# Performance work log

Hardware: AMD Instinct MI355X
Metric: run time of the kernel (lower is better)

Reference implementation:

```python
import jax, jax.numpy as jnp
import numpy as np


def _cubic_coeffs(t):
    # Catmull-Rom-style weights used by the original bicubic_interpolate
    t2 = t * t
    t3 = t2 * t
    cm1 = (-t3 + 2.0 * t2 - t) / 2.0
    c0 = (3.0 * t3 - 5.0 * t2 + 2.0) / 2.0
    c1 = (-3.0 * t3 + 4.0 * t2 + t) / 2.0
    c2 = 1.0 - (cm1 + c0 + c1)
    return (cm1, c0, c1, c2)


def _warp_bicubic(input_image, delta_x, delta_y):
    B, C, H, W = input_image.shape
    BXC = B * C
    # identity meshgrid, normalized to [-1, 1] then mapped back (faithful to source)
    gx = jnp.arange(W, dtype=jnp.float32)[None, None, :]   # [1,1,W]
    gy = jnp.arange(H, dtype=jnp.float32)[None, :, None]   # [1,H,1]
    new_x = 2.0 * (gx + delta_x) / max(W - 1, 1) - 1.0     # [B,H,W]
    new_y = 2.0 * (gy + delta_y) / max(H - 1, 1) - 1.0
    # un-normalize to pixel coords; tile across channels exactly like X.repeat([C,1,1,1])
    x_map = jnp.tile((new_x + 1.0) * (W - 1) / 2.0, (C, 1, 1))  # [BXC,H,W]
    y_map = jnp.tile((new_y + 1.0) * (H - 1) / 2.0, (C, 1, 1))
    x0f = jnp.floor(x_map)
    y0f = jnp.floor(y_map)
    tx = x_map - x0f
    ty = y_map - y0f
    cx = _cubic_coeffs(tx)
    cy = _cubic_coeffs(ty)
    x0 = x0f.astype(jnp.int32)
    y0 = y0f.astype(jnp.int32)
    xs = [jnp.clip(x0 + o, 0, W - 1) for o in (-1, 0, 1, 2)]
    ys = [jnp.clip(y0 + o, 0, H - 1) for o in (-1, 0, 1, 2)]
    flat = input_image.reshape(-1)                          # b-major, c-minor
    base = (jnp.arange(BXC, dtype=jnp.int32) * (H * W))[:, None, None]
    out = jnp.zeros((BXC, H, W), dtype=jnp.float32)
    for i in range(4):
        row = jnp.zeros((BXC, H, W), dtype=jnp.float32)
        off_y = base + ys[i] * W
        for j in range(4):
            row = row + cx[j] * jnp.take(flat, off_y + xs[j])  # 16-tap gather
        out = out + cy[i] * row
    return out.reshape(B, C, H, W)


def setup_inputs() -> dict:
    key = jax.random.key(0)
    k1, k2, k3 = jax.random.split(key, 3)
    B, C, H, W = 8, 3, 1024, 1024
    return {
        "input_image": jax.random.normal(k1, (B, C, H, W), dtype=jnp.float32),
        "delta_x": jax.random.normal(k2, (B, H, W), dtype=jnp.float32),
        "delta_y": jax.random.normal(k3, (B, H, W), dtype=jnp.float32),
    }


def reference(input_image, delta_x, delta_y):
    # Warp_Object.forward with flag_bicubic_or_bilinear='bicubic',
    # delta maps shared across channels (3D delta branch).
    return _warp_bicubic(input_image, delta_x, delta_y)
```

## Files before the change

kernel.cpp:

```cpp
#include <hip/hip_runtime.h>
#include <hip/hip_fp16.h>


#define RTY 7
#define RWS 30
#define RTX 8
#define CLS 80
#define STR 82
#define NQ  (RWS * (CLS / 4))

struct alignas(8) Cell {
    __half2 a;
    __half2 b;
};
struct alignas(16) Cell2 { Cell c0, c1; };

__device__ __forceinline__ void cubic_coeffs(float t, float c[4]) {
    float t2 = t * t;
    float t3 = t2 * t;
    c[0] = (-t3 + 2.0f * t2 - t) * 0.5f;
    c[1] = (3.0f * t3 - 5.0f * t2 + 2.0f) * 0.5f;
    c[2] = (-3.0f * t3 + 4.0f * t2 + t) * 0.5f;
    c[3] = 1.0f - (c[0] + c[1] + c[2]);
}

__global__ __launch_bounds__(1024, 8) void warp_bicubic_kernel(
    const float* __restrict__ img,
    const float* __restrict__ dx,
    const float* __restrict__ dy,
    float* __restrict__ out,
    int B, int C, int H, int W)
{
    __shared__ Cell lds[RWS * STR];

    const int tx = threadIdx.x;
    const int ty = threadIdx.y;
    const int tid = ty * 64 + tx;
    const int X = blockIdx.x * 64;
    const int Y = blockIdx.y * 16;
    const int db = blockIdx.z;
    const int hw = H * W;

    const int x = X + tx;
    const int y = Y + ty;
    const int pos  = y * W + x;
    const int dofs = db * hw + pos;
    const float fdx = dx[dofs];
    const float fdy = dy[dofs];

    const float* __restrict__ ch0 = img + (size_t)db * hw;
    const float* __restrict__ ch1 = img + (size_t)(db + B) * hw;
    const float* __restrict__ ch2 = img + (size_t)(db + 2 * B) * hw;

    if (tid < NQ) {
        int r  = tid / 20;
        int qc = tid - r * 20;
        int gy  = Y - RTY + r;
        int gx0 = X - RTX + 4 * qc;
        Cell cells[4];
        if (gy >= 0 && gy < H && gx0 >= 0 && gx0 <= W - 4) {
            size_t off = (size_t)gy * W + gx0;
            float4 v0 = *(const float4*)(ch0 + off);
            float4 v1 = *(const float4*)(ch1 + off);
            float4 v2 = *(const float4*)(ch2 + off);
            cells[0].a = __floats2half2_rn(v0.x, v1.x);
            cells[0].b = __floats2half2_rn(v2.x, 0.0f);
            cells[1].a = __floats2half2_rn(v0.y, v1.y);
            cells[1].b = __floats2half2_rn(v2.y, 0.0f);
            cells[2].a = __floats2half2_rn(v0.z, v1.z);
            cells[2].b = __floats2half2_rn(v2.z, 0.0f);
            cells[3].a = __floats2half2_rn(v0.w, v1.w);
            cells[3].b = __floats2half2_rn(v2.w, 0.0f);
        } else {
            int gyc = min(max(gy, 0), H - 1);
#pragma unroll
            for (int e = 0; e < 4; ++e) {
                int gxc = min(max(gx0 + e, 0), W - 1);
                size_t off = (size_t)gyc * W + gxc;
                cells[e].a = __floats2half2_rn(ch0[off], ch1[off]);
                cells[e].b = __floats2half2_rn(ch2[off], 0.0f);
            }
        }
        Cell2* dst = (Cell2*)&lds[r * STR + 4 * qc];
        dst[0] = *(const Cell2*)&cells[0];
        dst[1] = *(const Cell2*)&cells[2];
    }
    __syncthreads();

    const float xm = (float)x + fdx;
    const float ym = (float)y + fdy;
    const float x0f = floorf(xm);
    const float y0f = floorf(ym);
    const float tfx = xm - x0f;
    const float tfy = ym - y0f;

    float cx[4], cy[4];
    cubic_coeffs(tfx, cx);
    cubic_coeffs(tfy, cy);

    const int x0 = (int)x0f;
    const int y0 = (int)y0f;

    float a0, a1, a2;

    const unsigned ulx = (unsigned)(x0 - X + (RTX - 1));
    const unsigned uly = (unsigned)(y0 - Y + (RTY - 1));

    if (ulx <= (unsigned)(CLS - 4) && uly <= (unsigned)(RWS - 4)) {
        const Cell* __restrict__ base = lds + uly * STR + ulx;
        __half2 cxh[4], cyh[4];
#pragma unroll
        for (int j = 0; j < 4; ++j) {
            cxh[j] = __float2half2_rn(cx[j]);
            cyh[j] = __float2half2_rn(cy[j]);
        }
        __half2 acc01 = __float2half2_rn(0.0f);
        __half2 acc2  = __float2half2_rn(0.0f);
#pragma unroll
        for (int i = 0; i < 4; ++i) {
            const Cell* __restrict__ row = base + i * STR;
            Cell t0 = row[0];
            Cell t1 = row[1];
            Cell t2 = row[2];
            Cell t3 = row[3];
            __half2 r01 = __hmul2(cxh[0], t0.a);
            r01 = __hfma2(cxh[1], t1.a, r01);
            r01 = __hfma2(cxh[2], t2.a, r01);
            r01 = __hfma2(cxh[3], t3.a, r01);
            __half2 r2 = __hmul2(cxh[0], t0.b);
            r2 = __hfma2(cxh[1], t1.b, r2);
            r2 = __hfma2(cxh[2], t2.b, r2);
            r2 = __hfma2(cxh[3], t3.b, r2);
            acc01 = __hfma2(cyh[i], r01, acc01);
            acc2  = __hfma2(cyh[i], r2, acc2);
        }
        a0 = __low2float(acc01);
        a1 = __high2float(acc01);
        a2 = __low2float(acc2);
    } else {
        a0 = a1 = a2 = 0.0f;
        int xs[4], rowoff[4];
#pragma unroll
        for (int o = 0; o < 4; ++o) {
            xs[o] = min(max(x0 - 1 + o, 0), W - 1);
            rowoff[o] = min(max(y0 - 1 + o, 0), H - 1) * W;
        }
#pragma unroll
        for (int i = 0; i < 4; ++i) {
            float w0 = cy[i] * cx[0], w1 = cy[i] * cx[1];
            float w2 = cy[i] * cx[2], w3 = cy[i] * cx[3];
            const float* r0 = ch0 + rowoff[i];
            const float* r1 = ch1 + rowoff[i];
            const float* r2 = ch2 + rowoff[i];
            a0 = fmaf(w0, r0[xs[0]], a0); a0 = fmaf(w1, r0[xs[1]], a0);
            a0 = fmaf(w2, r0[xs[2]], a0); a0 = fmaf(w3, r0[xs[3]], a0);
            a1 = fmaf(w0, r1[xs[0]], a1); a1 = fmaf(w1, r1[xs[1]], a1);
            a1 = fmaf(w2, r1[xs[2]], a1); a1 = fmaf(w3, r1[xs[3]], a1);
            a2 = fmaf(w0, r2[xs[0]], a2); a2 = fmaf(w1, r2[xs[1]], a2);
            a2 = fmaf(w2, r2[xs[2]], a2); a2 = fmaf(w3, r2[xs[3]], a2);
        }
    }

    out[(size_t)db * hw + pos] = a0;
    out[(size_t)(db + B) * hw + pos] = a1;
    out[(size_t)(db + 2 * B) * hw + pos] = a2;
}

extern "C" void kernel_launch(void* const* d_in, const int* in_sizes, int n_in,
                              void* d_out, int out_size, void* d_ws, size_t ws_size,
                              hipStream_t stream) {
    const float* img = (const float*)d_in[0];
    const float* dx  = (const float*)d_in[1];
    const float* dy  = (const float*)d_in[2];
    float* out = (float*)d_out;

    const int B = 8, C = 3, H = 1024, W = 1024;
    dim3 block(64, 16, 1);
    dim3 grid(W / 64, H / 16, B);
    warp_bicubic_kernel<<<grid, block, 0, stream>>>(img, dx, dy, out, B, C, H, W);
}
```

Before: 63.64 us.

## Make blocks persistent over vertical tiles with double-buffered LDS prefetch

Each block now processes 8 consecutive 16-row tiles instead of one. It double-buffers the shared-memory halo tile and prefetches the next tile's image rows and displacement values into registers while the current tile is computed. The goal is to hide global load latency behind the LDS stencil math. The cost is fewer blocks (1024 instead of 8192), more registers, and a sync per tile, which may reduce occupancy and parallelism. Halo rows still get reloaded for each tile, so there is no cross-tile reuse.

```diff
diff --git a/kernel.cpp b/kernel.cpp
--- a/kernel.cpp
+++ b/kernel.cpp
@@ -2,6 +2,8 @@
 #include <hip/hip_fp16.h>
 
 
+#define TLH 16
+#define TPB 8
 #define RTY 7
 #define RWS 30
 #define RTX 8
@@ -31,139 +33,178 @@
     float* __restrict__ out,
     int B, int C, int H, int W)
 {
-    __shared__ Cell lds[RWS * STR];
+    __shared__ Cell lds[2][RWS * STR];
 
     const int tx = threadIdx.x;
     const int ty = threadIdx.y;
     const int tid = ty * 64 + tx;
-    const int X = blockIdx.x * 64;
-    const int Y = blockIdx.y * 16;
+    const int X  = blockIdx.x * 64;
+    const int Y0 = blockIdx.y * (TLH * TPB);
     const int db = blockIdx.z;
     const int hw = H * W;
-
-    const int x = X + tx;
-    const int y = Y + ty;
-    const int pos  = y * W + x;
-    const int dofs = db * hw + pos;
-    const float fdx = dx[dofs];
-    const float fdy = dy[dofs];
 
     const float* __restrict__ ch0 = img + (size_t)db * hw;
     const float* __restrict__ ch1 = img + (size_t)(db + B) * hw;
     const float* __restrict__ ch2 = img + (size_t)(db + 2 * B) * hw;
 
-    if (tid < NQ) {
-        int r  = tid / 20;
-        int qc = tid - r * 20;
-        int gy  = Y - RTY + r;
-        int gx0 = X - RTX + 4 * qc;
-        Cell cells[4];
-        if (gy >= 0 && gy < H && gx0 >= 0 && gx0 <= W - 4) {
-            size_t off = (size_t)gy * W + gx0;
-            float4 v0 = *(const float4*)(ch0 + off);
-            float4 v1 = *(const float4*)(ch1 + off);
-            float4 v2 = *(const float4*)(ch2 + off);
-            cells[0].a = __floats2half2_rn(v0.x, v1.x);
-            cells[0].b = __floats2half2_rn(v2.x, 0.0f);
-            cells[1].a = __floats2half2_rn(v0.y, v1.y);
-            cells[1].b = __floats2half2_rn(v2.y, 0.0f);
-            cells[2].a = __floats2half2_rn(v0.z, v1.z);
-            cells[2].b = __floats2half2_rn(v2.z, 0.0f);
-            cells[3].a = __floats2half2_rn(v0.w, v1.w);
-            cells[3].b = __floats2half2_rn(v2.w, 0.0f);
+    const int x = X + tx;
+
+    const bool sact = tid < NQ;
+    const int sr   = tid / 20;
+    const int sqc  = tid - sr * 20;
+    const int sgx0 = X - RTX + 4 * sqc;
+
+    float4 v0, v1, v2;
+    float fdx_n, fdy_n;
+
+    auto issue_delta = [&](int t) {
+        int y = Y0 + t * TLH + ty;
+        int dofs = db * hw + y * W + x;
+        fdx_n = dx[dofs];
+        fdy_n = dy[dofs];
+    };
+
+    auto issue_stage = [&](int t) {
+        if (!sact) return;
+        int gy = Y0 + t * TLH - RTY + sr;
+        if (gy >= 0 && gy < H && sgx0 >= 0 && sgx0 <= W - 4) {
+            size_t off = (size_t)gy * W + sgx0;
+            v0 = *(const float4*)(ch0 + off);
+            v1 = *(const float4*)(ch1 + off);
+            v2 = *(const float4*)(ch2 + off);
         } else {
             int gyc = min(max(gy, 0), H - 1);
+            float e0[4], e1[4], e2[4];
 #pragma unroll
             for (int e = 0; e < 4; ++e) {
-                int gxc = min(max(gx0 + e, 0), W - 1);
+                int gxc = min(max(sgx0 + e, 0), W - 1);
                 size_t off = (size_t)gyc * W + gxc;
-                cells[e].a = __floats2half2_rn(ch0[off], ch1[off]);
-                cells[e].b = __floats2half2_rn(ch2[off], 0.0f);
-            }
-        }
-        Cell2* dst = (Cell2*)&lds[r * STR + 4 * qc];
+                e0[e] = ch0[off]; e1[e] = ch1[off]; e2[e] = ch2[off];
+            }
+            v0 = make_float4(e0[0], e0[1], e0[2], e0[3]);
+            v1 = make_float4(e1[0], e1[1], e1[2], e1[3]);
+            v2 = make_float4(e2[0], e2[1], e2[2], e2[3]);
+        }
+    };
+
+    auto write_stage = [&](int buf) {
+        if (!sact) return;
+        Cell cells[4];
+        cells[0].a = __floats2half2_rn(v0.x, v1.x);
+        cells[0].b = __floats2half2_rn(v2.x, 0.0f);
+        cells[1].a = __floats2half2_rn(v0.y, v1.y);
+        cells[1].b = __floats2half2_rn(v2.y, 0.0f);
+        cells[2].a = __floats2half2_rn(v0.z, v1.z);
+        cells[2].b = __floats2half2_rn(v2.z, 0.0f);
+        cells[3].a = __floats2half2_rn(v0.w, v1.w);
+        cells[3].b = __floats2half2_rn(v2.w, 0.0f);
+        Cell2* dst = (Cell2*)&lds[buf][sr * STR + 4 * sqc];
         dst[0] = *(const Cell2*)&cells[0];
         dst[1] = *(const Cell2*)&cells[2];
+    };
+
+    auto compute_tile = [&](int t, int buf, float fdx, float fdy) {
+        const int Yt = Y0 + t * TLH;
+        const int y = Yt + ty;
+        const int pos = y * W + x;
+
+        const float xm = (float)x + fdx;
+        const float ym = (float)y + fdy;
+        const float x0f = floorf(xm);
+        const float y0f = floorf(ym);
+        const float tfx = xm - x0f;
+        const float tfy = ym - y0f;
+
+        float cx[4], cy[4];
+        cubic_coeffs(tfx, cx);
+        cubic_coeffs(tfy, cy);
+
+        const int x0 = (int)x0f;
+        const int y0 = (int)y0f;
+
+        float a0, a1, a2;
+
+        const unsigned ulx = (unsigned)(x0 - X + (RTX - 1));
+        const unsigned uly = (unsigned)(y0 - Yt + (RTY - 1));
+
+        if (ulx <= (unsigned)(CLS - 4) && uly <= (unsigned)(RWS - 4)) {
+            const Cell* __restrict__ base = &lds[buf][uly * STR + ulx];
+            __half2 cxh[4], cyh[4];
+#pragma unroll
+            for (int j = 0; j < 4; ++j) {
+                cxh[j] = __float2half2_rn(cx[j]);
+                cyh[j] = __float2half2_rn(cy[j]);
+            }
+            __half2 acc01 = __float2half2_rn(0.0f);
+            __half2 acc2  = __float2half2_rn(0.0f);
+#pragma unroll
+            for (int i = 0; i < 4; ++i) {
+                const Cell* __restrict__ row = base + i * STR;
+                Cell t0 = row[0];
+                Cell t1 = row[1];
+                Cell t2 = row[2];
+                Cell t3 = row[3];
+                __half2 r01 = __hmul2(cxh[0], t0.a);
+                r01 = __hfma2(cxh[1], t1.a, r01);
+                r01 = __hfma2(cxh[2], t2.a, r01);
+                r01 = __hfma2(cxh[3], t3.a, r01);
+                __half2 r2 = __hmul2(cxh[0], t0.b);
+                r2 = __hfma2(cxh[1], t1.b, r2);
+                r2 = __hfma2(cxh[2], t2.b, r2);
+                r2 = __hfma2(cxh[3], t3.b, r2);
+                acc01 = __hfma2(cyh[i], r01, acc01);
+                acc2  = __hfma2(cyh[i], r2, acc2);
+            }
+            a0 = __low2float(acc01);
+            a1 = __high2float(acc01);
+            a2 = __low2float(acc2);
+        } else {
+            a0 = a1 = a2 = 0.0f;
+            int xs[4], rowoff[4];
+#pragma unroll
+            for (int o = 0; o < 4; ++o) {
+                xs[o] = min(max(x0 - 1 + o, 0), W - 1);
+                rowoff[o] = min(max(y0 - 1 + o, 0), H - 1) * W;
+            }
+#pragma unroll
+            for (int i = 0; i < 4; ++i) {
+                float w0 = cy[i] * cx[0], w1 = cy[i] * cx[1];
+                float w2 = cy[i] * cx[2], w3 = cy[i] * cx[3];
+                const float* r0 = ch0 + rowoff[i];
+                const float* r1 = ch1 + rowoff[i];
+                const float* r2 = ch2 + rowoff[i];
+                a0 = fmaf(w0, r0[xs[0]], a0); a0 = fmaf(w1, r0[xs[1]], a0);
+                a0 = fmaf(w2, r0[xs[2]], a0); a0 = fmaf(w3, r0[xs[3]], a0);
+                a1 = fmaf(w0, r1[xs[0]], a1); a1 = fmaf(w1, r1[xs[1]], a1);
+                a1 = fmaf(w2, r1[xs[2]], a1); a1 = fmaf(w3, r1[xs[3]], a1);
+                a2 = fmaf(w0, r2[xs[0]], a2); a2 = fmaf(w1, r2[xs[1]], a2);
+                a2 = fmaf(w2, r2[xs[2]], a2); a2 = fmaf(w3, r2[xs[3]], a2);
+            }
+        }
+
+        out[(size_t)db * hw + pos] = a0;
+        out[(size_t)(db + B) * hw + pos] = a1;
+        out[(size_t)(db + 2 * B) * hw + pos] = a2;
+    };
+
+    issue_delta(0);
+    issue_stage(0);
+    write_stage(0);
+    __syncthreads();
+
+    for (int t = 0; t < TPB; ++t) {
+        const float fdx = fdx_n;
+        const float fdy = fdy_n;
+        if (t + 1 < TPB) {
+            issue_delta(t + 1);
+            issue_stage(t + 1);
+        }
+        compute_tile(t, t & 1, fdx, fdy);
+        if (t + 1 < TPB) {
+            write_stage((t + 1) & 1);
+        }
+        __syncthreads();
     }
-    __syncthreads();
-
-    const float xm = (float)x + fdx;
-    const float ym = (float)y + fdy;
-    const float x0f = floorf(xm);
-    const float y0f = floorf(ym);
-    const float tfx = xm - x0f;
-    const float tfy = ym - y0f;
-
-    float cx[4], cy[4];
-    cubic_coeffs(tfx, cx);
-    cubic_coeffs(tfy, cy);
-
-    const int x0 = (int)x0f;
-    const int y0 = (int)y0f;
-
-    float a0, a1, a2;
-
-    const unsigned ulx = (unsigned)(x0 - X + (RTX - 1));
-    const unsigned uly = (unsigned)(y0 - Y + (RTY - 1));
-
-    if (ulx <= (unsigned)(CLS - 4) && uly <= (unsigned)(RWS - 4)) {
-        const Cell* __restrict__ base = lds + uly * STR + ulx;
-        __half2 cxh[4], cyh[4];
-#pragma unroll
-        for (int j = 0; j < 4; ++j) {
-            cxh[j] = __float2half2_rn(cx[j]);
-            cyh[j] = __float2half2_rn(cy[j]);
-        }
-        __half2 acc01 = __float2half2_rn(0.0f);
-        __half2 acc2  = __float2half2_rn(0.0f);
-#pragma unroll
-        for (int i = 0; i < 4; ++i) {
-            const Cell* __restrict__ row = base + i * STR;
-            Cell t0 = row[0];
-            Cell t1 = row[1];
-            Cell t2 = row[2];
-            Cell t3 = row[3];
-            __half2 r01 = __hmul2(cxh[0], t0.a);
-            r01 = __hfma2(cxh[1], t1.a, r01);
-            r01 = __hfma2(cxh[2], t2.a, r01);
-            r01 = __hfma2(cxh[3], t3.a, r01);
-            __half2 r2 = __hmul2(cxh[0], t0.b);
-            r2 = __hfma2(cxh[1], t1.b, r2);
-            r2 = __hfma2(cxh[2], t2.b, r2);
-            r2 = __hfma2(cxh[3], t3.b, r2);
-            acc01 = __hfma2(cyh[i], r01, acc01);
-            acc2  = __hfma2(cyh[i], r2, acc2);
-        }
-        a0 = __low2float(acc01);
-        a1 = __high2float(acc01);
-        a2 = __low2float(acc2);
-    } else {
-        a0 = a1 = a2 = 0.0f;
-        int xs[4], rowoff[4];
-#pragma unroll
-        for (int o = 0; o < 4; ++o) {
-            xs[o] = min(max(x0 - 1 + o, 0), W - 1);
-            rowoff[o] = min(max(y0 - 1 + o, 0), H - 1) * W;
-        }
-#pragma unroll
-        for (int i = 0; i < 4; ++i) {
-            float w0 = cy[i] * cx[0], w1 = cy[i] * cx[1];
-            float w2 = cy[i] * cx[2], w3 = cy[i] * cx[3];
-            const float* r0 = ch0 + rowoff[i];
-            const float* r1 = ch1 + rowoff[i];
-            const float* r2 = ch2 + rowoff[i];
-            a0 = fmaf(w0, r0[xs[0]], a0); a0 = fmaf(w1, r0[xs[1]], a0);
-            a0 = fmaf(w2, r0[xs[2]], a0); a0 = fmaf(w3, r0[xs[3]], a0);
-            a1 = fmaf(w0, r1[xs[0]], a1); a1 = fmaf(w1, r1[xs[1]], a1);
-            a1 = fmaf(w2, r1[xs[2]], a1); a1 = fmaf(w3, r1[xs[3]], a1);
-            a2 = fmaf(w0, r2[xs[0]], a2); a2 = fmaf(w1, r2[xs[1]], a2);
-            a2 = fmaf(w2, r2[xs[2]], a2); a2 = fmaf(w3, r2[xs[3]], a2);
-        }
-    }
-
-    out[(size_t)db * hw + pos] = a0;
-    out[(size_t)(db + B) * hw + pos] = a1;
-    out[(size_t)(db + 2 * B) * hw + pos] = a2;
 }
 
 extern "C" void kernel_launch(void* const* d_in, const int* in_sizes, int n_in,
@@ -176,6 +217,6 @@
 
     const int B = 8, C = 3, H = 1024, W = 1024;
     dim3 block(64, 16, 1);
-    dim3 grid(W / 64, H / 16, B);
+    dim3 grid(W / 64, H / (TLH * TPB), B);
     warp_bicubic_kernel<<<grid, block, 0, stream>>>(img, dx, dy, out, B, C, H, W);
 }
```

After: 112.4 us. 76.7% more time.

## Split LDS tile into channel-pair plane and overlapping-pair plane for third channel

Applied to the files above, without the earlier changes.

The shared-memory tile changes from 8-byte cells (ch0/ch1 pair plus ch2 padded with zero) to two 4-byte planes. One plane holds ch0/ch1 pairs, the other holds adjacent ch2 pixel pairs (x, x+1). The third channel then needs only two half2 loads and two packed FMAs per row instead of four, with a final horizontal add. This cuts LDS traffic and half-precision ALU work in the hot path, at the cost of one extra global load per staging thread and a changed fast-path boundary condition for the staging load.

```diff
diff --git a/kernel.cpp b/kernel.cpp
--- a/kernel.cpp
+++ b/kernel.cpp
@@ -6,14 +6,9 @@
 #define RWS 30
 #define RTX 8
 #define CLS 80
-#define STR 82
+#define SA  84
+#define PB  (RWS * SA)
 #define NQ  (RWS * (CLS / 4))
-
-struct alignas(8) Cell {
-    __half2 a;
-    __half2 b;
-};
-struct alignas(16) Cell2 { Cell c0, c1; };
 
 __device__ __forceinline__ void cubic_coeffs(float t, float c[4]) {
     float t2 = t * t;
@@ -24,6 +19,11 @@
     c[3] = 1.0f - (c[0] + c[1] + c[2]);
 }
 
+__device__ __forceinline__ unsigned pack2(float a, float b) {
+    __half2 h = __floats2half2_rn(a, b);
+    return *reinterpret_cast<unsigned*>(&h);
+}
+
 __global__ __launch_bounds__(1024, 8) void warp_bicubic_kernel(
     const float* __restrict__ img,
     const float* __restrict__ dx,
@@ -31,7 +31,7 @@
     float* __restrict__ out,
     int B, int C, int H, int W)
 {
-    __shared__ Cell lds[RWS * STR];
+    __shared__ unsigned lds[2 * RWS * SA];
 
     const int tx = threadIdx.x;
     const int ty = threadIdx.y;
@@ -56,34 +56,40 @@
         int r  = tid / 20;
         int qc = tid - r * 20;
         int gy  = Y - RTY + r;
+        int gyc = min(max(gy, 0), H - 1);
+        size_t rowb = (size_t)gyc * W;
         int gx0 = X - RTX + 4 * qc;
-        Cell cells[4];
-        if (gy >= 0 && gy < H && gx0 >= 0 && gx0 <= W - 4) {
-            size_t off = (size_t)gy * W + gx0;
-            float4 v0 = *(const float4*)(ch0 + off);
-            float4 v1 = *(const float4*)(ch1 + off);
-            float4 v2 = *(const float4*)(ch2 + off);
-            cells[0].a = __floats2half2_rn(v0.x, v1.x);
-            cells[0].b = __floats2half2_rn(v2.x, 0.0f);
-            cells[1].a = __floats2half2_rn(v0.y, v1.y);
-            cells[1].b = __floats2half2_rn(v2.y, 0.0f);
-            cells[2].a = __floats2half2_rn(v0.z, v1.z);
-            cells[2].b = __floats2half2_rn(v2.z, 0.0f);
-            cells[3].a = __floats2half2_rn(v0.w, v1.w);
-            cells[3].b = __floats2half2_rn(v2.w, 0.0f);
+        float4 v0, v1, v2;
+        float v2e;
+        if (gx0 >= 0 && gx0 + 4 <= W - 1) {
+            v0 = *(const float4*)(ch0 + rowb + gx0);
+            v1 = *(const float4*)(ch1 + rowb + gx0);
+            v2 = *(const float4*)(ch2 + rowb + gx0);
+            v2e = ch2[rowb + gx0 + 4];
         } else {
-            int gyc = min(max(gy, 0), H - 1);
-#pragma unroll
-            for (int e = 0; e < 4; ++e) {
-                int gxc = min(max(gx0 + e, 0), W - 1);
-                size_t off = (size_t)gyc * W + gxc;
-                cells[e].a = __floats2half2_rn(ch0[off], ch1[off]);
-                cells[e].b = __floats2half2_rn(ch2[off], 0.0f);
-            }
+            int g0 = min(max(gx0    , 0), W - 1);
+            int g1 = min(max(gx0 + 1, 0), W - 1);
+            int g2 = min(max(gx0 + 2, 0), W - 1);
+            int g3 = min(max(gx0 + 3, 0), W - 1);
+            int g4 = min(max(gx0 + 4, 0), W - 1);
+            v0 = make_float4(ch0[rowb + g0], ch0[rowb + g1], ch0[rowb + g2], ch0[rowb + g3]);
+            v1 = make_float4(ch1[rowb + g0], ch1[rowb + g1], ch1[rowb + g2], ch1[rowb + g3]);
+            v2 = make_float4(ch2[rowb + g0], ch2[rowb + g1], ch2[rowb + g2], ch2[rowb + g3]);
+            v2e = ch2[rowb + g4];
         }
-        Cell2* dst = (Cell2*)&lds[r * STR + 4 * qc];
-        dst[0] = *(const Cell2*)&cells[0];
-        dst[1] = *(const Cell2*)&cells[2];
+        uint4 ua;
+        ua.x = pack2(v0.x, v1.x);
+        ua.y = pack2(v0.y, v1.y);
+        ua.z = pack2(v0.z, v1.z);
+        ua.w = pack2(v0.w, v1.w);
+        uint4 ub;
+        ub.x = pack2(v2.x, v2.y);
+        ub.y = pack2(v2.y, v2.z);
+        ub.z = pack2(v2.z, v2.w);
+        ub.w = pack2(v2.w, v2e);
+        const int cell = r * SA + 4 * qc;
+        *(uint4*)&lds[cell] = ua;
+        *(uint4*)&lds[PB + cell] = ub;
     }
     __syncthreads();
 
@@ -107,36 +113,44 @@
     const unsigned uly = (unsigned)(y0 - Y + (RTY - 1));
 
     if (ulx <= (unsigned)(CLS - 4) && uly <= (unsigned)(RWS - 4)) {
-        const Cell* __restrict__ base = lds + uly * STR + ulx;
+        const int ib = (int)uly * SA + (int)ulx;
+        const __half2* __restrict__ LA = (const __half2*)&lds[ib];
+        const __half2* __restrict__ LB = (const __half2*)&lds[PB + ib];
+
         __half2 cxh[4], cyh[4];
 #pragma unroll
         for (int j = 0; j < 4; ++j) {
             cxh[j] = __float2half2_rn(cx[j]);
             cyh[j] = __float2half2_rn(cy[j]);
         }
+        const __half2 pw0 = __halves2half2(__float2half(cx[0]), __float2half(cx[1]));
+        const __half2 pw1 = __halves2half2(__float2half(cx[2]), __float2half(cx[3]));
+
         __half2 acc01 = __float2half2_rn(0.0f);
-        __half2 acc2  = __float2half2_rn(0.0f);
+        __half2 acc2v = __float2half2_rn(0.0f);
 #pragma unroll
         for (int i = 0; i < 4; ++i) {
-            const Cell* __restrict__ row = base + i * STR;
-            Cell t0 = row[0];
-            Cell t1 = row[1];
-            Cell t2 = row[2];
-            Cell t3 = row[3];
-            __half2 r01 = __hmul2(cxh[0], t0.a);
-            r01 = __hfma2(cxh[1], t1.a, r01);
-            r01 = __hfma2(cxh[2], t2.a, r01);
-            r01 = __hfma2(cxh[3], t3.a, r01);
-            __half2 r2 = __hmul2(cxh[0], t0.b);
-            r2 = __hfma2(cxh[1], t1.b, r2);
-            r2 = __hfma2(cxh[2], t2.b, r2);
-            r2 = __hfma2(cxh[3], t3.b, r2);
+            const __half2* __restrict__ rA = LA + i * SA;
+            const __half2* __restrict__ rB = LB + i * SA;
+            __half2 a0t = rA[0];
+            __half2 a1t = rA[1];
+            __half2 a2t = rA[2];
+            __half2 a3t = rA[3];
+            __half2 r01 = __hmul2(cxh[0], a0t);
+            r01 = __hfma2(cxh[1], a1t, r01);
+            r01 = __hfma2(cxh[2], a2t, r01);
+            r01 = __hfma2(cxh[3], a3t, r01);
             acc01 = __hfma2(cyh[i], r01, acc01);
-            acc2  = __hfma2(cyh[i], r2, acc2);
+
+            __half2 b0t = rB[0];
+            __half2 b1t = rB[2];
+            __half2 r2 = __hmul2(pw0, b0t);
+            r2 = __hfma2(pw1, b1t, r2);
+            acc2v = __hfma2(cyh[i], r2, acc2v);
         }
         a0 = __low2float(acc01);
         a1 = __high2float(acc01);
-        a2 = __low2float(acc2);
+        a2 = __low2float(acc2v) + __high2float(acc2v);
     } else {
         a0 = a1 = a2 = 0.0f;
         int xs[4], rowoff[4];
```

Result: slower. 87.68 us (+37.8%).

## Process two output rows per thread with a taller shared-memory halo tile

Applied to the files above, without the earlier changes.

Each 64x16 block now covers a 64x32 output tile. Every thread computes two pixels 16 rows apart, and the staged LDS region grows from 30 to 46 rows, so the halo rows are loaded relatively fewer times. The staging loader is also simplified: it always clamps rows and only falls back to scalar loads at the x edges. The cost is half as many blocks, more LDS per block (which may reduce occupancy), and a serial two-pixel loop per thread.

```diff
diff --git a/kernel.cpp b/kernel.cpp
--- a/kernel.cpp
+++ b/kernel.cpp
@@ -3,7 +3,7 @@
 
 
 #define RTY 7
-#define RWS 30
+#define RWS 46
 #define RTX 8
 #define CLS 80
 #define STR 82
@@ -37,16 +37,20 @@
     const int ty = threadIdx.y;
     const int tid = ty * 64 + tx;
     const int X = blockIdx.x * 64;
-    const int Y = blockIdx.y * 16;
+    const int Y = blockIdx.y * 32;
     const int db = blockIdx.z;
     const int hw = H * W;
 
     const int x = X + tx;
-    const int y = Y + ty;
-    const int pos  = y * W + x;
-    const int dofs = db * hw + pos;
-    const float fdx = dx[dofs];
-    const float fdy = dy[dofs];
+
+    float fdxs[2], fdys[2];
+#pragma unroll
+    for (int p = 0; p < 2; ++p) {
+        int yy = Y + ty + p * 16;
+        int dofs = db * hw + yy * W + x;
+        fdxs[p] = dx[dofs];
+        fdys[p] = dy[dofs];
+    }
 
     const float* __restrict__ ch0 = img + (size_t)db * hw;
     const float* __restrict__ ch1 = img + (size_t)(db + B) * hw;
@@ -56,114 +60,121 @@
         int r  = tid / 20;
         int qc = tid - r * 20;
         int gy  = Y - RTY + r;
+        int gyc = min(max(gy, 0), H - 1);
+        size_t rowb = (size_t)gyc * W;
         int gx0 = X - RTX + 4 * qc;
-        Cell cells[4];
-        if (gy >= 0 && gy < H && gx0 >= 0 && gx0 <= W - 4) {
-            size_t off = (size_t)gy * W + gx0;
-            float4 v0 = *(const float4*)(ch0 + off);
-            float4 v1 = *(const float4*)(ch1 + off);
-            float4 v2 = *(const float4*)(ch2 + off);
-            cells[0].a = __floats2half2_rn(v0.x, v1.x);
-            cells[0].b = __floats2half2_rn(v2.x, 0.0f);
-            cells[1].a = __floats2half2_rn(v0.y, v1.y);
-            cells[1].b = __floats2half2_rn(v2.y, 0.0f);
-            cells[2].a = __floats2half2_rn(v0.z, v1.z);
-            cells[2].b = __floats2half2_rn(v2.z, 0.0f);
-            cells[3].a = __floats2half2_rn(v0.w, v1.w);
-            cells[3].b = __floats2half2_rn(v2.w, 0.0f);
+        float4 v0, v1, v2;
+        if (gx0 >= 0 && gx0 <= W - 4) {
+            v0 = *(const float4*)(ch0 + rowb + gx0);
+            v1 = *(const float4*)(ch1 + rowb + gx0);
+            v2 = *(const float4*)(ch2 + rowb + gx0);
         } else {
-            int gyc = min(max(gy, 0), H - 1);
-#pragma unroll
-            for (int e = 0; e < 4; ++e) {
-                int gxc = min(max(gx0 + e, 0), W - 1);
-                size_t off = (size_t)gyc * W + gxc;
-                cells[e].a = __floats2half2_rn(ch0[off], ch1[off]);
-                cells[e].b = __floats2half2_rn(ch2[off], 0.0f);
-            }
+            int g0 = min(max(gx0    , 0), W - 1);
+            int g1 = min(max(gx0 + 1, 0), W - 1);
+            int g2 = min(max(gx0 + 2, 0), W - 1);
+            int g3 = min(max(gx0 + 3, 0), W - 1);
+            v0 = make_float4(ch0[rowb + g0], ch0[rowb + g1], ch0[rowb + g2], ch0[rowb + g3]);
+            v1 = make_float4(ch1[rowb + g0], ch1[rowb + g1], ch1[rowb + g2], ch1[rowb + g3]);
+            v2 = make_float4(ch2[rowb + g0], ch2[rowb + g1], ch2[rowb + g2], ch2[rowb + g3]);
         }
+        Cell c0, c1, c2, c3;
+        c0.a = __floats2half2_rn(v0.x, v1.x); c0.b = __floats2half2_rn(v2.x, 0.0f);
+        c1.a = __floats2half2_rn(v0.y, v1.y); c1.b = __floats2half2_rn(v2.y, 0.0f);
+        c2.a = __floats2half2_rn(v0.z, v1.z); c2.b = __floats2half2_rn(v2.z, 0.0f);
+        c3.a = __floats2half2_rn(v0.w, v1.w); c3.b = __floats2half2_rn(v2.w, 0.0f);
+        Cell2 q0; q0.c0 = c0; q0.c1 = c1;
+        Cell2 q1; q1.c0 = c2; q1.c1 = c3;
         Cell2* dst = (Cell2*)&lds[r * STR + 4 * qc];
-        dst[0] = *(const Cell2*)&cells[0];
-        dst[1] = *(const Cell2*)&cells[2];
+        dst[0] = q0;
+        dst[1] = q1;
     }
     __syncthreads();
 
-    const float xm = (float)x + fdx;
-    const float ym = (float)y + fdy;
-    const float x0f = floorf(xm);
-    const float y0f = floorf(ym);
-    const float tfx = xm - x0f;
-    const float tfy = ym - y0f;
+#pragma unroll
+    for (int p = 0; p < 2; ++p) {
+        const int y = Y + ty + p * 16;
+        const int pos = y * W + x;
+        const float fdx = fdxs[p];
+        const float fdy = fdys[p];
 
-    float cx[4], cy[4];
-    cubic_coeffs(tfx, cx);
-    cubic_coeffs(tfy, cy);
+        const float xm = (float)x + fdx;
+        const float ym = (float)y + fdy;
+        const float x0f = floorf(xm);
+        const float y0f = floorf(ym);
+        const float tfx = xm - x0f;
+        const float tfy = ym - y0f;
 
-    const int x0 = (int)x0f;
-    const int y0 = (int)y0f;
+        float cx[4], cy[4];
+        cubic_coeffs(tfx, cx);
+        cubic_coeffs(tfy, cy);
 
-    float a0, a1, a2;
+        const int x0 = (int)x0f;
+        const int y0 = (int)y0f;
 
-    const unsigned ulx = (unsigned)(x0 - X + (RTX - 1));
-    const unsigned uly = (unsigned)(y0 - Y + (RTY - 1));
+        float a0, a1, a2;
 
-    if (ulx <= (unsigned)(CLS - 4) && uly <= (unsigned)(RWS - 4)) {
-        const Cell* __restrict__ base = lds + uly * STR + ulx;
-        __half2 cxh[4], cyh[4];
+        const unsigned ulx = (unsigned)(x0 - X + (RTX - 1));
+        const unsigned uly = (unsigned)(y0 - Y + (RTY - 1));
+
+        if (ulx <= (unsigned)(CLS - 4) && uly <= (unsigned)(RWS - 4)) {
+            const Cell* __restrict__ base = lds + uly * STR + ulx;
+            __half2 cxh[4], cyh[4];
 #pragma unroll
-        for (int j = 0; j < 4; ++j) {
-            cxh[j] = __float2half2_rn(cx[j]);
-            cyh[j] = __float2half2_rn(cy[j]);
+            for (int j = 0; j < 4; ++j) {
+                cxh[j] = __float2half2_rn(cx[j]);
+                cyh[j] = __float2half2_rn(cy[j]);
+            }
+            __half2 acc01 = __float2half2_rn(0.0f);
+            __half2 acc2  = __float2half2_rn(0.0f);
+#pragma unroll
+            for (int i = 0; i < 4; ++i) {
+                const Cell* __restrict__ row = base + i * STR;
+                Cell t0 = row[0];
+                Cell t1 = row[1];
+                Cell t2 = row[2];
+                Cell t3 = row[3];
+                __half2 r01 = __hmul2(cxh[0], t0.a);
+                r01 = __hfma2(cxh[1], t1.a, r01);
+                r01 = __hfma2(cxh[2], t2.a, r01);
+                r01 = __hfma2(cxh[3], t3.a, r01);
+                __half2 r2 = __hmul2(cxh[0], t0.b);
+                r2 = __hfma2(cxh[1], t1.b, r2);
+                r2 = __hfma2(cxh[2], t2.b, r2);
+                r2 = __hfma2(cxh[3], t3.b, r2);
+                acc01 = __hfma2(cyh[i], r01, acc01);
+                acc2  = __hfma2(cyh[i], r2, acc2);
+            }
+            a0 = __low2float(acc01);
+            a1 = __high2float(acc01);
+            a2 = __low2float(acc2);
+        } else {
+            a0 = a1 = a2 = 0.0f;
+            int xs[4], rowoff[4];
+#pragma unroll
+            for (int o = 0; o < 4; ++o) {
+                xs[o] = min(max(x0 - 1 + o, 0), W - 1);
+                rowoff[o] = min(max(y0 - 1 + o, 0), H - 1) * W;
+            }
+#pragma unroll
+            for (int i = 0; i < 4; ++i) {
+                float w0 = cy[i] * cx[0], w1 = cy[i] * cx[1];
+                float w2 = cy[i] * cx[2], w3 = cy[i] * cx[3];
+                const float* r0 = ch0 + rowoff[i];
+                const float* r1 = ch1 + rowoff[i];
+                const float* r2 = ch2 + rowoff[i];
+                a0 = fmaf(w0, r0[xs[0]], a0); a0 = fmaf(w1, r0[xs[1]], a0);
+                a0 = fmaf(w2, r0[xs[2]], a0); a0 = fmaf(w3, r0[xs[3]], a0);
+                a1 = fmaf(w0, r1[xs[0]], a1); a1 = fmaf(w1, r1[xs[1]], a1);
+                a1 = fmaf(w2, r1[xs[2]], a1); a1 = fmaf(w3, r1[xs[3]], a1);
+                a2 = fmaf(w0, r2[xs[0]], a2); a2 = fmaf(w1, r2[xs[1]], a2);
+                a2 = fmaf(w2, r2[xs[2]], a2); a2 = fmaf(w3, r2[xs[3]], a2);
+            }
         }
-        __half2 acc01 = __float2half2_rn(0.0f);
-        __half2 acc2  = __float2half2_rn(0.0f);
-#pragma unroll
-        for (int i = 0; i < 4; ++i) {
-            const Cell* __restrict__ row = base + i * STR;
-            Cell t0 = row[0];
-            Cell t1 = row[1];
-            Cell t2 = row[2];
-            Cell t3 = row[3];
-            __half2 r01 = __hmul2(cxh[0], t0.a);
-            r01 = __hfma2(cxh[1], t1.a, r01);
-            r01 = __hfma2(cxh[2], t2.a, r01);
-            r01 = __hfma2(cxh[3], t3.a, r01);
-            __half2 r2 = __hmul2(cxh[0], t0.b);
-            r2 = __hfma2(cxh[1], t1.b, r2);
-            r2 = __hfma2(cxh[2], t2.b, r2);
-            r2 = __hfma2(cxh[3], t3.b, r2);
-            acc01 = __hfma2(cyh[i], r01, acc01);
-            acc2  = __hfma2(cyh[i], r2, acc2);
-        }
-        a0 = __low2float(acc01);
-        a1 = __high2float(acc01);
-        a2 = __low2float(acc2);
-    } else {
-        a0 = a1 = a2 = 0.0f;
-        int xs[4], rowoff[4];
-#pragma unroll
-        for (int o = 0; o < 4; ++o) {
-            xs[o] = min(max(x0 - 1 + o, 0), W - 1);
-            rowoff[o] = min(max(y0 - 1 + o, 0), H - 1) * W;
-        }
-#pragma unroll
-        for (int i = 0; i < 4; ++i) {
-            float w0 = cy[i] * cx[0], w1 = cy[i] * cx[1];
-            float w2 = cy[i] * cx[2], w3 = cy[i] * cx[3];
-            const float* r0 = ch0 + rowoff[i];
-            const float* r1 = ch1 + rowoff[i];
-            const float* r2 = ch2 + rowoff[i];
-            a0 = fmaf(w0, r0[xs[0]], a0); a0 = fmaf(w1, r0[xs[1]], a0);
-            a0 = fmaf(w2, r0[xs[2]], a0); a0 = fmaf(w3, r0[xs[3]], a0);
-            a1 = fmaf(w0, r1[xs[0]], a1); a1 = fmaf(w1, r1[xs[1]], a1);
-            a1 = fmaf(w2, r1[xs[2]], a1); a1 = fmaf(w3, r1[xs[3]], a1);
-            a2 = fmaf(w0, r2[xs[0]], a2); a2 = fmaf(w1, r2[xs[1]], a2);
-            a2 = fmaf(w2, r2[xs[2]], a2); a2 = fmaf(w3, r2[xs[3]], a2);
-        }
+
+        out[(size_t)db * hw + pos] = a0;
+        out[(size_t)(db + B) * hw + pos] = a1;
+        out[(size_t)(db + 2 * B) * hw + pos] = a2;
     }
-
-    out[(size_t)db * hw + pos] = a0;
-    out[(size_t)(db + B) * hw + pos] = a1;
-    out[(size_t)(db + 2 * B) * hw + pos] = a2;
 }
 
 extern "C" void kernel_launch(void* const* d_in, const int* in_sizes, int n_in,
@@ -176,6 +187,6 @@
 
     const int B = 8, C = 3, H = 1024, W = 1024;
     dim3 block(64, 16, 1);
-    dim3 grid(W / 64, H / 16, B);
+    dim3 grid(W / 64, H / 32, B);
     warp_bicubic_kernel<<<grid, block, 0, stream>>>(img, dx, dy, out, B, C, H, W);
 }
```

New measurement: 70.03 us. 1.1x slower.
